# Performance work log

Hardware: AMD Instinct MI355X
Metric: run time of the kernel (lower is better)

Reference implementation:

```python
import jax, jax.numpy as jnp
import numpy as np

B, S, D, H = 1, 2048, 1024, 16
HD = D // H
FF = 4 * D
EPS_LN = 1e-5
EPS_ATTN = 1e-6


def _layernorm(x, g, b):
    mu = jnp.mean(x, axis=-1, keepdims=True)
    var = jnp.mean(jnp.square(x - mu), axis=-1, keepdims=True)
    return (x - mu) * jax.lax.rsqrt(var + EPS_LN) * g + b


def setup_inputs() -> dict:
    key = jax.random.key(0)
    ks = jax.random.split(key, 12)
    w = lambda k, shape: (jax.random.normal(k, shape, jnp.float32) * 0.02)
    return {
        "x": jax.random.normal(ks[0], (B, S, D), jnp.float32),
        "Wq": w(ks[1], (D, D)), "bq": jnp.zeros((D,), jnp.float32),
        "Wk": w(ks[2], (D, D)), "bk": jnp.zeros((D,), jnp.float32),
        "Wv": w(ks[3], (D, D)), "bv": jnp.zeros((D,), jnp.float32),
        "Wo": w(ks[4], (D, D)), "bo": jnp.zeros((D,), jnp.float32),
        "W1": w(ks[5], (FF, D)), "bb1": jnp.zeros((FF,), jnp.float32),
        "W2": w(ks[6], (D, FF)), "bb2": jnp.zeros((D,), jnp.float32),
        "g1": jnp.ones((D,), jnp.float32), "be1": jnp.zeros((D,), jnp.float32),
        "g2": jnp.ones((D,), jnp.float32), "be2": jnp.zeros((D,), jnp.float32),
    }


def reference(x, Wq, bq, Wk, bk, Wv, bv, Wo, bo, W1, bb1, W2, bb2, g1, be1, g2, be2):
    # --- pre-norm causal linear attention ---
    h = _layernorm(x, g1, be1)                     # (B,S,D)
    def heads(t):
        return t.reshape(B, S, H, HD).transpose(0, 2, 1, 3)  # (B,H,S,hd)
    q = heads(h @ Wq.T + bq)
    k = heads(h @ Wk.T + bk)
    v = heads(h @ Wv.T + bv)
    # feature map phi(x) = elu(x) + 1 (strictly positive)
    q = jax.nn.elu(q) + 1.0
    k = jax.nn.elu(k) + 1.0
    # causal cumulative state: S_t = sum_{i<=t} k_i v_i^T ; z_t = sum_{i<=t} k_i
    kv = jnp.cumsum(jnp.einsum("bhsd,bhse->bhsde", k, v), axis=2)  # (B,H,S,hd,hd)
    z = jnp.cumsum(k, axis=2)                                       # (B,H,S,hd)
    num = jnp.einsum("bhsd,bhsde->bhse", q, kv)                    # (B,H,S,hd)
    den = jnp.einsum("bhsd,bhsd->bhs", q, z) + EPS_ATTN
    attn = (num / den[..., None]).transpose(0, 2, 1, 3).reshape(B, S, D)
    attn = attn @ Wo.T + bo
    x = x + attn
    # --- FFN (GELU exact, matching torch nn.GELU default) ---
    h2 = _layernorm(x, g2, be2)
    ff = jax.nn.gelu(h2 @ W1.T + bb1, approximate=False) @ W2.T + bb2
    return x + ff
```

## Files before the change

kernel.cpp:

```cpp
#include <hip/hip_runtime.h>
#include <hip/hip_bf16.h>
#include <math.h>

constexpr int S  = 2048;
constexpr int D  = 1024;
constexpr int H  = 16;
constexpr int HD = 64;
constexpr int FF = 4096;
constexpr int NC  = 32;
constexpr int CHK = 64;
constexpr int QS  = 3 * D;

typedef __attribute__((ext_vector_type(8))) short bf16x8;
typedef __attribute__((ext_vector_type(4))) float f32x4;

__device__ inline unsigned short f2bf(float f) {
    unsigned int u = __float_as_uint(f);
    u = (u + 0x7FFFu + ((u >> 16) & 1u)) >> 16;
    return (unsigned short)u;
}

__global__ __launch_bounds__(256) void cvt_bf16(const float* __restrict__ src,
                                                unsigned short* __restrict__ dst,
                                                int n4) {
    int i = blockIdx.x * 256 + threadIdx.x;
    if (i >= n4) return;
    float4 v = ((const float4*)src)[i];
    ushort4 o = { f2bf(v.x), f2bf(v.y), f2bf(v.z), f2bf(v.w) };
    ((ushort4*)dst)[i] = o;
}

__global__ __launch_bounds__(256) void concat3(const float* __restrict__ a,
                                               const float* __restrict__ b,
                                               const float* __restrict__ c,
                                               float* __restrict__ o) {
    int i = blockIdx.x * 256 + threadIdx.x;
    if (i >= 3 * D) return;
    const float* s = (i < D) ? a : ((i < 2 * D) ? b : c);
    o[i] = s[i & (D - 1)];
}

__global__ __launch_bounds__(256) void layernorm_bf16(const float* __restrict__ x,
                                                      const float* __restrict__ g,
                                                      const float* __restrict__ b,
                                                      unsigned short* __restrict__ out) {
    const int row = blockIdx.x, tid = threadIdx.x;
    float4 v = ((const float4*)(x + (size_t)row * D))[tid];
    float s  = v.x + v.y + v.z + v.w;
    float ss = v.x*v.x + v.y*v.y + v.z*v.z + v.w*v.w;
    #pragma unroll
    for (int off = 32; off > 0; off >>= 1) {
        s  += __shfl_down(s, off);
        ss += __shfl_down(ss, off);
    }
    __shared__ float sw[4], ssw[4];
    if ((tid & 63) == 0) { sw[tid >> 6] = s; ssw[tid >> 6] = ss; }
    __syncthreads();
    s  = sw[0] + sw[1] + sw[2] + sw[3];
    ss = ssw[0] + ssw[1] + ssw[2] + ssw[3];
    const float mu = s * (1.0f / D);
    const float rs = rsqrtf(ss * (1.0f / D) - mu * mu + 1e-5f);
    float4 gv = ((const float4*)g)[tid];
    float4 bv = ((const float4*)b)[tid];
    ushort4 o = { f2bf((v.x - mu) * rs * gv.x + bv.x),
                  f2bf((v.y - mu) * rs * gv.y + bv.y),
                  f2bf((v.z - mu) * rs * gv.z + bv.z),
                  f2bf((v.w - mu) * rs * gv.w + bv.w) };
    ((ushort4*)(out + (size_t)row * D))[tid] = o;
}

enum { EPI_F32 = 0, EPI_QKV = 1, EPI_GELU_BF16 = 2, EPI_PART = 3 };

template <int EPI>
__global__ __launch_bounds__(256) void gemm_bt(const unsigned short* __restrict__ A,
                                               const unsigned short* __restrict__ W,
                                               const float* __restrict__ bias,
                                               void* __restrict__ outp,
                                               int M, int N, int K, int kSplit) {
    __shared__ unsigned short As[128 * 32];
    __shared__ unsigned short Bs[128 * 32];
    const int tid  = threadIdx.x;
    const int tileM = blockIdx.x * 128;
    const int tileN = blockIdx.y * 128;
    const int w    = tid >> 6, lane = tid & 63;
    const int wm   = (w >> 1) * 64, wn = (w & 1) * 64;
    const int lr   = lane & 15, lk = lane >> 4;
    const int kLen   = K / kSplit;
    const int kStart = blockIdx.z * kLen;
    const int kEnd   = kStart + kLen;

    f32x4 acc[4][4];
    #pragma unroll
    for (int i = 0; i < 4; ++i)
        #pragma unroll
        for (int j = 0; j < 4; ++j) acc[i][j] = (f32x4)(0.0f);

    for (int k0 = kStart; k0 < kEnd; k0 += 32) {
        #pragma unroll
        for (int p = 0; p < 2; ++p) {
            const int c   = p * 256 + tid;
            const int row = c >> 2, kc = (c & 3) * 8;
            __builtin_amdgcn_global_load_lds(
                (const __attribute__((address_space(1))) unsigned int*)
                    (A + (size_t)(tileM + row) * K + k0 + kc),
                (__attribute__((address_space(3))) unsigned int*)&As[c * 8],
                16, 0, 0);
            __builtin_amdgcn_global_load_lds(
                (const __attribute__((address_space(1))) unsigned int*)
                    (W + (size_t)(tileN + row) * K + k0 + kc),
                (__attribute__((address_space(3))) unsigned int*)&Bs[c * 8],
                16, 0, 0);
        }
        __syncthreads();
        bf16x8 af[4], bfv[4];
        #pragma unroll
        for (int i = 0; i < 4; ++i) {
            af[i]  = *(const bf16x8*)&As[(wm + i * 16 + lr) * 32 + lk * 8];
            bfv[i] = *(const bf16x8*)&Bs[(wn + i * 16 + lr) * 32 + lk * 8];
        }
        #pragma unroll
        for (int i = 0; i < 4; ++i)
            #pragma unroll
            for (int j = 0; j < 4; ++j)
                acc[i][j] = __builtin_amdgcn_mfma_f32_16x16x32_bf16(af[i], bfv[j], acc[i][j], 0, 0, 0);
        __syncthreads();
    }

    #pragma unroll
    for (int i = 0; i < 4; ++i) {
        const int rbase = tileM + wm + i * 16 + lk * 4;
        #pragma unroll
        for (int j = 0; j < 4; ++j) {
            const int col = tileN + wn + j * 16 + lr;
            #pragma unroll
            for (int r = 0; r < 4; ++r) {
                const int row = rbase + r;
                const size_t off = (size_t)row * N + col;
                float v = acc[i][j][r];
                if constexpr (EPI == EPI_PART) {
                    ((float*)outp)[(size_t)blockIdx.z * (size_t)M * (size_t)N + off] = v;
                } else if constexpr (EPI == EPI_QKV) {
                    v += bias[col];
                    if (col < 2 * D) v = v > 0.0f ? v + 1.0f : __expf(v);
                    ((float*)outp)[off] = v;
                } else if constexpr (EPI == EPI_GELU_BF16) {
                    v += bias[col];
                    float gl = 0.5f * v * (1.0f + erff(v * 0.70710678118654752f));
                    ((unsigned short*)outp)[off] = f2bf(gl);
                } else {
                    v += bias[col];
                    ((float*)outp)[off] = v;
                }
            }
        }
    }
}

__global__ __launch_bounds__(256) void reduce_bias_res(const float* __restrict__ part,
                                                       const float* __restrict__ bias,
                                                       const float* __restrict__ res,
                                                       float* __restrict__ out,
                                                       int N4, int total4, int KS) {
    int i = blockIdx.x * 256 + threadIdx.x;
    if (i >= total4) return;
    float4 a = ((const float4*)part)[i];
    for (int z = 1; z < KS; ++z) {
        float4 p = ((const float4*)part)[(size_t)z * total4 + i];
        a.x += p.x; a.y += p.y; a.z += p.z; a.w += p.w;
    }
    float4 b = ((const float4*)bias)[i % N4];
    float4 r = ((const float4*)res)[i];
    a.x += b.x + r.x; a.y += b.y + r.y; a.z += b.z + r.z; a.w += b.w + r.w;
    ((float4*)out)[i] = a;
}

__global__ __launch_bounds__(256) void attn_chunk_sums(const float* __restrict__ qkv,
                                                       float* __restrict__ KVc,
                                                       float* __restrict__ Zc) {
    const int c = blockIdx.x, h = blockIdx.y, tid = threadIdx.x;
    __shared__ float Kc[CHK * HD], Vc[CHK * HD];
    const int s0 = c * CHK;
    #pragma unroll
    for (int p = 0; p < 4; ++p) {
        int cc = p * 256 + tid;
        int t = cc >> 4, dp = (cc & 15) * 4;
        *(float4*)&Kc[t * HD + dp] = *(const float4*)(qkv + (size_t)(s0 + t) * QS + D     + h * HD + dp);
        *(float4*)&Vc[t * HD + dp] = *(const float4*)(qkv + (size_t)(s0 + t) * QS + 2 * D + h * HD + dp);
    }
    __syncthreads();
    const int d = tid >> 2, e0 = (tid & 3) * 16;
    float acc[16];
    #pragma unroll
    for (int j = 0; j < 16; ++j) acc[j] = 0.0f;
    float zacc = 0.0f;
    for (int t = 0; t < CHK; ++t) {
        float kv = Kc[t * HD + d];
        zacc += kv;
        #pragma unroll
        for (int j = 0; j < 16; ++j) acc[j] += kv * Vc[t * HD + e0 + j];
    }
    float* op = KVc + ((size_t)(h * NC + c) * HD + d) * HD + e0;
    #pragma unroll
    for (int j = 0; j < 16; ++j) op[j] = acc[j];
    if ((tid & 3) == 0) Zc[(size_t)(h * NC + c) * HD + d] = zacc;
}

__global__ __launch_bounds__(256) void attn_prefix(float* __restrict__ KVc,
                                                   float* __restrict__ Zc) {
    const int h = blockIdx.y;
    const int elem = blockIdx.x * 256 + threadIdx.x;
    size_t base = (size_t)h * NC * (HD * HD) + elem;
    float run = 0.0f;
    for (int c = 0; c < NC; ++c) {
        float t = KVc[base + (size_t)c * (HD * HD)];
        KVc[base + (size_t)c * (HD * HD)] = run;
        run += t;
    }
    if (blockIdx.x == 0 && threadIdx.x < HD) {
        size_t zb = (size_t)h * NC * HD + threadIdx.x;
        float zr = 0.0f;
        for (int c = 0; c < NC; ++c) {
            float t = Zc[zb + (size_t)c * HD];
            Zc[zb + (size_t)c * HD] = zr;
            zr += t;
        }
    }
}

__global__ __launch_bounds__(256) void attn_out(const float* __restrict__ qkv,
                                                const float* __restrict__ KVpre,
                                                const float* __restrict__ Zpre,
                                                unsigned short* __restrict__ attn) {
    const int c = blockIdx.x, h = blockIdx.y, tid = threadIdx.x;
    __shared__ float Qc[CHK * HD], KVs[CHK * HD], Pre[HD * HD], Sc[CHK * CHK];
    __shared__ float zp[HD], den[CHK];
    const int s0 = c * CHK;
    #pragma unroll
    for (int p = 0; p < 4; ++p) {
        int cc = p * 256 + tid;
        int t = cc >> 4, dp = (cc & 15) * 4;
        *(float4*)&Qc[t * HD + dp]  = *(const float4*)(qkv + (size_t)(s0 + t) * QS +     h * HD + dp);
        *(float4*)&KVs[t * HD + dp] = *(const float4*)(qkv + (size_t)(s0 + t) * QS + D + h * HD + dp);
        ((float4*)Pre)[cc] = *(const float4*)(KVpre + (size_t)(h * NC + c) * (HD * HD) + cc * 4);
    }
    if (tid < HD) zp[tid] = Zpre[(size_t)(h * NC + c) * HD + tid];
    __syncthreads();

    const int tt = tid >> 2, i0 = (tid & 3) * 16;
    for (int i = i0; i < i0 + 16; ++i) {
        float sv = 0.0f;
        for (int d2 = 0; d2 < HD; ++d2) sv += Qc[tt * HD + d2] * KVs[i * HD + d2];
        Sc[tt * CHK + i] = (i <= tt) ? sv : 0.0f;
    }
    __syncthreads();

    if (tid < CHK) {
        float dv = 1e-6f;
        for (int d2 = 0; d2 < HD; ++d2) dv += Qc[tid * HD + d2] * zp[d2];
        for (int i = 0; i < CHK; ++i) dv += Sc[tid * CHK + i];
        den[tid] = dv;
    }
    #pragma unroll
    for (int p = 0; p < 4; ++p) {
        int cc = p * 256 + tid;
        int t = cc >> 4, dp = (cc & 15) * 4;
        *(float4*)&KVs[t * HD + dp] = *(const float4*)(qkv + (size_t)(s0 + t) * QS + 2 * D + h * HD + dp);
    }
    __syncthreads();

    float o[16];
    #pragma unroll
    for (int j = 0; j < 16; ++j) o[j] = 0.0f;
    for (int d2 = 0; d2 < HD; ++d2) {
        float qv = Qc[tt * HD + d2];
        float sv = Sc[tt * CHK + d2];
        #pragma unroll
        for (int j = 0; j < 16; ++j)
            o[j] += qv * Pre[d2 * HD + i0 + j] + sv * KVs[d2 * HD + i0 + j];
    }
    const float inv = 1.0f / den[tt];
    unsigned short* op = attn + (size_t)(s0 + tt) * D + h * HD + i0;
    #pragma unroll
    for (int j0 = 0; j0 < 16; j0 += 4) {
        ushort4 ov = { f2bf(o[j0] * inv), f2bf(o[j0 + 1] * inv),
                       f2bf(o[j0 + 2] * inv), f2bf(o[j0 + 3] * inv) };
        *(ushort4*)(op + j0) = ov;
    }
}

extern "C" void kernel_launch(void* const* d_in, const int* in_sizes, int n_in,
                              void* d_out, int out_size, void* d_ws, size_t ws_size,
                              hipStream_t stream) {
    const float* x   = (const float*)d_in[0];
    const float* Wq  = (const float*)d_in[1];
    const float* bq  = (const float*)d_in[2];
    const float* Wk  = (const float*)d_in[3];
    const float* bk  = (const float*)d_in[4];
    const float* Wv  = (const float*)d_in[5];
    const float* bv  = (const float*)d_in[6];
    const float* Wo  = (const float*)d_in[7];
    const float* bo  = (const float*)d_in[8];
    const float* W1  = (const float*)d_in[9];
    const float* b1  = (const float*)d_in[10];
    const float* W2  = (const float*)d_in[11];
    const float* b2  = (const float*)d_in[12];
    const float* g1  = (const float*)d_in[13];
    const float* be1 = (const float*)d_in[14];
    const float* g2  = (const float*)d_in[15];
    const float* be2 = (const float*)d_in[16];
    float* out = (float*)d_out;

    char* wsp = (char*)d_ws;
    auto alloc = [&](size_t bytes) {
        char* p = wsp;
        wsp += (bytes + 255) & ~(size_t)255;
        return p;
    };
    unsigned short* h1   = (unsigned short*)alloc((size_t)S * D * 2);
    unsigned short* attn = (unsigned short*)alloc((size_t)S * D * 2);
    unsigned short* gbuf = (unsigned short*)alloc((size_t)S * FF * 2);
    float* x2   = (float*)alloc((size_t)S * D * 4);
    unsigned short* Wqkvb = (unsigned short*)alloc((size_t)3 * D * D * 2);
    unsigned short* Wob   = (unsigned short*)alloc((size_t)D * D * 2);
    unsigned short* W1b   = (unsigned short*)alloc((size_t)FF * D * 2);
    unsigned short* W2b   = (unsigned short*)alloc((size_t)D * FF * 2);
    float* bqkv = (float*)alloc((size_t)3 * D * 4);
    float* KVc  = (float*)alloc((size_t)H * NC * HD * HD * 4);
    float* Zc   = (float*)alloc((size_t)H * NC * HD * 4);
    char* uni = (char*)alloc((size_t)32 * 1024 * 1024);
    float* qkv   = (float*)uni;
    float* parts = (float*)uni;

    const int DD4 = D * D / 4, FD4 = FF * D / 4;
    cvt_bf16<<<DD4 / 256, 256, 0, stream>>>(Wq, Wqkvb,             DD4);
    cvt_bf16<<<DD4 / 256, 256, 0, stream>>>(Wk, Wqkvb + D * D,     DD4);
    cvt_bf16<<<DD4 / 256, 256, 0, stream>>>(Wv, Wqkvb + 2 * D * D, DD4);
    cvt_bf16<<<DD4 / 256, 256, 0, stream>>>(Wo, Wob, DD4);
    cvt_bf16<<<FD4 / 256, 256, 0, stream>>>(W1, W1b, FD4);
    cvt_bf16<<<FD4 / 256, 256, 0, stream>>>(W2, W2b, FD4);
    concat3<<<(3 * D + 255) / 256, 256, 0, stream>>>(bq, bk, bv, bqkv);

    layernorm_bf16<<<S, 256, 0, stream>>>(x, g1, be1, h1);

    gemm_bt<EPI_QKV><<<dim3(S / 128, 3 * D / 128, 1), 256, 0, stream>>>(
        h1, Wqkvb, bqkv, qkv, S, 3 * D, D, 1);

    attn_chunk_sums<<<dim3(NC, H), 256, 0, stream>>>(qkv, KVc, Zc);
    attn_prefix<<<dim3(16, H), 256, 0, stream>>>(KVc, Zc);
    attn_out<<<dim3(NC, H), 256, 0, stream>>>(qkv, KVc, Zc, attn);

    gemm_bt<EPI_PART><<<dim3(S / 128, D / 128, 2), 256, 0, stream>>>(
        attn, Wob, nullptr, parts, S, D, D, 2);
    reduce_bias_res<<<(S * D / 4 + 255) / 256, 256, 0, stream>>>(
        parts, bo, x, x2, D / 4, S * D / 4, 2);

    layernorm_bf16<<<S, 256, 0, stream>>>(x2, g2, be2, h1);

    gemm_bt<EPI_GELU_BF16><<<dim3(S / 128, FF / 128, 1), 256, 0, stream>>>(
        h1, W1b, b1, gbuf, S, FF, D, 1);

    gemm_bt<EPI_PART><<<dim3(S / 128, D / 128, 4), 256, 0, stream>>>(
        gbuf, W2b, nullptr, parts, S, D, FF, 4);
    reduce_bias_res<<<(S * D / 4 + 255) / 256, 256, 0, stream>>>(
        parts, b2, x2, out, D / 4, S * D / 4, 4);
}
```

Measured before the change: 319.5 us.

## Merge weight conversions, fuse residual reduce with layernorm, use 512-thread GEMM blocks

Six weight-conversion launches and the bias concat are replaced by one kernel, and the QKV bias is now chosen per column in the epilogue. The split-K reduce after the output projection is fused with the second layernorm, which removes one kernel and one pass over x2. The GEMM moves to 512 threads in 8 waves, each wave owning a 64x32 sub-tile, which halves accumulator registers and lets each thread issue one LDS load per operand. Launch overhead and memory traffic drop, but per-wave MFMA work is smaller, so A-fragment reuse per wave is lower.

```diff
diff --git a/kernel.cpp b/kernel.cpp
--- a/kernel.cpp
+++ b/kernel.cpp
@@ -20,24 +20,33 @@
     return (unsigned short)u;
 }
 
-__global__ __launch_bounds__(256) void cvt_bf16(const float* __restrict__ src,
-                                                unsigned short* __restrict__ dst,
-                                                int n4) {
+constexpr int DD4 = D * D / 4;
+constexpr int FD4 = FF * D / 4;
+constexpr int CVT_TOTAL4 = 4 * DD4 + 2 * FD4;
+
+__global__ __launch_bounds__(256) void cvt6(const float* __restrict__ Wq,
+                                            const float* __restrict__ Wk,
+                                            const float* __restrict__ Wv,
+                                            const float* __restrict__ Wo,
+                                            const float* __restrict__ W1,
+                                            const float* __restrict__ W2,
+                                            unsigned short* __restrict__ Wqkvb,
+                                            unsigned short* __restrict__ Wob,
+                                            unsigned short* __restrict__ W1b,
+                                            unsigned short* __restrict__ W2b) {
     int i = blockIdx.x * 256 + threadIdx.x;
-    if (i >= n4) return;
-    float4 v = ((const float4*)src)[i];
+    if (i >= CVT_TOTAL4) return;
+    const float* s;
+    unsigned short* dp;
+    if (i < DD4)                 { s = Wq + (size_t)i * 4;               dp = Wqkvb + (size_t)i * 4; }
+    else if (i < 2 * DD4)        { s = Wk + (size_t)(i - DD4) * 4;       dp = Wqkvb + (size_t)i * 4; }
+    else if (i < 3 * DD4)        { s = Wv + (size_t)(i - 2 * DD4) * 4;   dp = Wqkvb + (size_t)i * 4; }
+    else if (i < 4 * DD4)        { s = Wo + (size_t)(i - 3 * DD4) * 4;   dp = Wob + (size_t)(i - 3 * DD4) * 4; }
+    else if (i < 4 * DD4 + FD4)  { s = W1 + (size_t)(i - 4 * DD4) * 4;   dp = W1b + (size_t)(i - 4 * DD4) * 4; }
+    else                         { s = W2 + (size_t)(i - 4 * DD4 - FD4) * 4; dp = W2b + (size_t)(i - 4 * DD4 - FD4) * 4; }
+    float4 v = *(const float4*)s;
     ushort4 o = { f2bf(v.x), f2bf(v.y), f2bf(v.z), f2bf(v.w) };
-    ((ushort4*)dst)[i] = o;
-}
-
-__global__ __launch_bounds__(256) void concat3(const float* __restrict__ a,
-                                               const float* __restrict__ b,
-                                               const float* __restrict__ c,
-                                               float* __restrict__ o) {
-    int i = blockIdx.x * 256 + threadIdx.x;
-    if (i >= 3 * D) return;
-    const float* s = (i < D) ? a : ((i < 2 * D) ? b : c);
-    o[i] = s[i & (D - 1)];
+    *(ushort4*)dp = o;
 }
 
 __global__ __launch_bounds__(256) void layernorm_bf16(const float* __restrict__ x,
@@ -69,59 +78,121 @@
     ((ushort4*)(out + (size_t)row * D))[tid] = o;
 }
 
+template <int KS>
+__global__ __launch_bounds__(256) void reduce_ln(const float* __restrict__ part,
+                                                 const float* __restrict__ bias,
+                                                 const float* __restrict__ res,
+                                                 float* __restrict__ x2,
+                                                 const float* __restrict__ g,
+                                                 const float* __restrict__ b,
+                                                 unsigned short* __restrict__ out) {
+    const int row = blockIdx.x, tid = threadIdx.x;
+    const size_t i4 = (size_t)row * 256 + tid;
+    float4 a = ((const float4*)part)[i4];
+    #pragma unroll
+    for (int z = 1; z < KS; ++z) {
+        float4 p = ((const float4*)part)[(size_t)z * S * 256 + i4];
+        a.x += p.x; a.y += p.y; a.z += p.z; a.w += p.w;
+    }
+    float4 bi = ((const float4*)bias)[tid];
+    float4 r  = ((const float4*)res)[i4];
+    a.x += bi.x + r.x; a.y += bi.y + r.y; a.z += bi.z + r.z; a.w += bi.w + r.w;
+    ((float4*)x2)[i4] = a;
+    float s  = a.x + a.y + a.z + a.w;
+    float ss = a.x*a.x + a.y*a.y + a.z*a.z + a.w*a.w;
+    #pragma unroll
+    for (int off = 32; off > 0; off >>= 1) {
+        s  += __shfl_down(s, off);
+        ss += __shfl_down(ss, off);
+    }
+    __shared__ float sw[4], ssw[4];
+    if ((tid & 63) == 0) { sw[tid >> 6] = s; ssw[tid >> 6] = ss; }
+    __syncthreads();
+    s  = sw[0] + sw[1] + sw[2] + sw[3];
+    ss = ssw[0] + ssw[1] + ssw[2] + ssw[3];
+    const float mu = s * (1.0f / D);
+    const float rs = rsqrtf(ss * (1.0f / D) - mu * mu + 1e-5f);
+    float4 gv = ((const float4*)g)[tid];
+    float4 bv = ((const float4*)b)[tid];
+    ushort4 o = { f2bf((a.x - mu) * rs * gv.x + bv.x),
+                  f2bf((a.y - mu) * rs * gv.y + bv.y),
+                  f2bf((a.z - mu) * rs * gv.z + bv.z),
+                  f2bf((a.w - mu) * rs * gv.w + bv.w) };
+    ((ushort4*)(out + (size_t)row * D))[tid] = o;
+}
+
+template <int KS>
+__global__ __launch_bounds__(256) void reduce_bias_res(const float* __restrict__ part,
+                                                       const float* __restrict__ bias,
+                                                       const float* __restrict__ res,
+                                                       float* __restrict__ out,
+                                                       int N4, int total4) {
+    int i = blockIdx.x * 256 + threadIdx.x;
+    if (i >= total4) return;
+    float4 a = ((const float4*)part)[i];
+    #pragma unroll
+    for (int z = 1; z < KS; ++z) {
+        float4 p = ((const float4*)part)[(size_t)z * total4 + i];
+        a.x += p.x; a.y += p.y; a.z += p.z; a.w += p.w;
+    }
+    float4 b = ((const float4*)bias)[i % N4];
+    float4 r = ((const float4*)res)[i];
+    a.x += b.x + r.x; a.y += b.y + r.y; a.z += b.z + r.z; a.w += b.w + r.w;
+    ((float4*)out)[i] = a;
+}
+
 enum { EPI_F32 = 0, EPI_QKV = 1, EPI_GELU_BF16 = 2, EPI_PART = 3 };
 
 template <int EPI>
-__global__ __launch_bounds__(256) void gemm_bt(const unsigned short* __restrict__ A,
-                                               const unsigned short* __restrict__ W,
-                                               const float* __restrict__ bias,
-                                               void* __restrict__ outp,
-                                               int M, int N, int K, int kSplit) {
+__global__ __launch_bounds__(512, 4) void gemm_bt(const unsigned short* __restrict__ A,
+                                                  const unsigned short* __restrict__ W,
+                                                  const float* __restrict__ bias,
+                                                  const float* __restrict__ bias2,
+                                                  const float* __restrict__ bias3,
+                                                  void* __restrict__ outp,
+                                                  int M, int N, int K, int kSplit) {
     __shared__ unsigned short As[128 * 32];
     __shared__ unsigned short Bs[128 * 32];
     const int tid  = threadIdx.x;
     const int tileM = blockIdx.x * 128;
     const int tileN = blockIdx.y * 128;
     const int w    = tid >> 6, lane = tid & 63;
-    const int wm   = (w >> 1) * 64, wn = (w & 1) * 64;
+    const int wm   = (w >> 2) * 64, wn = (w & 3) * 32;
     const int lr   = lane & 15, lk = lane >> 4;
     const int kLen   = K / kSplit;
     const int kStart = blockIdx.z * kLen;
     const int kEnd   = kStart + kLen;
-
-    f32x4 acc[4][4];
+    const int srow = tid >> 2, skc = (tid & 3) * 8;
+
+    f32x4 acc[4][2];
     #pragma unroll
     for (int i = 0; i < 4; ++i)
         #pragma unroll
-        for (int j = 0; j < 4; ++j) acc[i][j] = (f32x4)(0.0f);
+        for (int j = 0; j < 2; ++j) acc[i][j] = (f32x4)(0.0f);
 
     for (int k0 = kStart; k0 < kEnd; k0 += 32) {
-        #pragma unroll
-        for (int p = 0; p < 2; ++p) {
-            const int c   = p * 256 + tid;
-            const int row = c >> 2, kc = (c & 3) * 8;
-            __builtin_amdgcn_global_load_lds(
-                (const __attribute__((address_space(1))) unsigned int*)
-                    (A + (size_t)(tileM + row) * K + k0 + kc),
-                (__attribute__((address_space(3))) unsigned int*)&As[c * 8],
-                16, 0, 0);
-            __builtin_amdgcn_global_load_lds(
-                (const __attribute__((address_space(1))) unsigned int*)
-                    (W + (size_t)(tileN + row) * K + k0 + kc),
-                (__attribute__((address_space(3))) unsigned int*)&Bs[c * 8],
-                16, 0, 0);
-        }
+        __builtin_amdgcn_global_load_lds(
+            (const __attribute__((address_space(1))) unsigned int*)
+                (A + (size_t)(tileM + srow) * K + k0 + skc),
+            (__attribute__((address_space(3))) unsigned int*)&As[tid * 8],
+            16, 0, 0);
+        __builtin_amdgcn_global_load_lds(
+            (const __attribute__((address_space(1))) unsigned int*)
+                (W + (size_t)(tileN + srow) * K + k0 + skc),
+            (__attribute__((address_space(3))) unsigned int*)&Bs[tid * 8],
+            16, 0, 0);
         __syncthreads();
-        bf16x8 af[4], bfv[4];
-        #pragma unroll
-        for (int i = 0; i < 4; ++i) {
+        bf16x8 af[4], bfv[2];
+        #pragma unroll
+        for (int i = 0; i < 4; ++i)
             af[i]  = *(const bf16x8*)&As[(wm + i * 16 + lr) * 32 + lk * 8];
-            bfv[i] = *(const bf16x8*)&Bs[(wn + i * 16 + lr) * 32 + lk * 8];
-        }
+        #pragma unroll
+        for (int j = 0; j < 2; ++j)
+            bfv[j] = *(const bf16x8*)&Bs[(wn + j * 16 + lr) * 32 + lk * 8];
         #pragma unroll
         for (int i = 0; i < 4; ++i)
             #pragma unroll
-            for (int j = 0; j < 4; ++j)
+            for (int j = 0; j < 2; ++j)
                 acc[i][j] = __builtin_amdgcn_mfma_f32_16x16x32_bf16(af[i], bfv[j], acc[i][j], 0, 0, 0);
         __syncthreads();
     }
@@ -130,7 +201,7 @@
     for (int i = 0; i < 4; ++i) {
         const int rbase = tileM + wm + i * 16 + lk * 4;
         #pragma unroll
-        for (int j = 0; j < 4; ++j) {
+        for (int j = 0; j < 2; ++j) {
             const int col = tileN + wn + j * 16 + lr;
             #pragma unroll
             for (int r = 0; r < 4; ++r) {
@@ -140,7 +211,8 @@
                 if constexpr (EPI == EPI_PART) {
                     ((float*)outp)[(size_t)blockIdx.z * (size_t)M * (size_t)N + off] = v;
                 } else if constexpr (EPI == EPI_QKV) {
-                    v += bias[col];
+                    float bc = (col < D) ? bias[col] : ((col < 2 * D) ? bias2[col - D] : bias3[col - 2 * D]);
+                    v += bc;
                     if (col < 2 * D) v = v > 0.0f ? v + 1.0f : __expf(v);
                     ((float*)outp)[off] = v;
                 } else if constexpr (EPI == EPI_GELU_BF16) {
@@ -154,24 +226,6 @@
             }
         }
     }
-}
-
-__global__ __launch_bounds__(256) void reduce_bias_res(const float* __restrict__ part,
-                                                       const float* __restrict__ bias,
-                                                       const float* __restrict__ res,
-                                                       float* __restrict__ out,
-                                                       int N4, int total4, int KS) {
-    int i = blockIdx.x * 256 + threadIdx.x;
-    if (i >= total4) return;
-    float4 a = ((const float4*)part)[i];
-    for (int z = 1; z < KS; ++z) {
-        float4 p = ((const float4*)part)[(size_t)z * total4 + i];
-        a.x += p.x; a.y += p.y; a.z += p.z; a.w += p.w;
-    }
-    float4 b = ((const float4*)bias)[i % N4];
-    float4 r = ((const float4*)res)[i];
-    a.x += b.x + r.x; a.y += b.y + r.y; a.z += b.z + r.z; a.w += b.w + r.w;
-    ((float4*)out)[i] = a;
 }
 
 __global__ __launch_bounds__(256) void attn_chunk_sums(const float* __restrict__ qkv,
@@ -324,43 +378,33 @@
     unsigned short* Wob   = (unsigned short*)alloc((size_t)D * D * 2);
     unsigned short* W1b   = (unsigned short*)alloc((size_t)FF * D * 2);
     unsigned short* W2b   = (unsigned short*)alloc((size_t)D * FF * 2);
-    float* bqkv = (float*)alloc((size_t)3 * D * 4);
     float* KVc  = (float*)alloc((size_t)H * NC * HD * HD * 4);
     float* Zc   = (float*)alloc((size_t)H * NC * HD * 4);
     char* uni = (char*)alloc((size_t)32 * 1024 * 1024);
     float* qkv   = (float*)uni;
     float* parts = (float*)uni;
 
-    const int DD4 = D * D / 4, FD4 = FF * D / 4;
-    cvt_bf16<<<DD4 / 256, 256, 0, stream>>>(Wq, Wqkvb,             DD4);
-    cvt_bf16<<<DD4 / 256, 256, 0, stream>>>(Wk, Wqkvb + D * D,     DD4);
-    cvt_bf16<<<DD4 / 256, 256, 0, stream>>>(Wv, Wqkvb + 2 * D * D, DD4);
-    cvt_bf16<<<DD4 / 256, 256, 0, stream>>>(Wo, Wob, DD4);
-    cvt_bf16<<<FD4 / 256, 256, 0, stream>>>(W1, W1b, FD4);
-    cvt_bf16<<<FD4 / 256, 256, 0, stream>>>(W2, W2b, FD4);
-    concat3<<<(3 * D + 255) / 256, 256, 0, stream>>>(bq, bk, bv, bqkv);
+    cvt6<<<(CVT_TOTAL4 + 255) / 256, 256, 0, stream>>>(Wq, Wk, Wv, Wo, W1, W2,
+                                                       Wqkvb, Wob, W1b, W2b);
 
     layernorm_bf16<<<S, 256, 0, stream>>>(x, g1, be1, h1);
 
-    gemm_bt<EPI_QKV><<<dim3(S / 128, 3 * D / 128, 1), 256, 0, stream>>>(
-        h1, Wqkvb, bqkv, qkv, S, 3 * D, D, 1);
+    gemm_bt<EPI_QKV><<<dim3(S / 128, 3 * D / 128, 1), 512, 0, stream>>>(
+        h1, Wqkvb, bq, bk, bv, qkv, S, 3 * D, D, 1);
 
     attn_chunk_sums<<<dim3(NC, H), 256, 0, stream>>>(qkv, KVc, Zc);
     attn_prefix<<<dim3(16, H), 256, 0, stream>>>(KVc, Zc);
     attn_out<<<dim3(NC, H), 256, 0, stream>>>(qkv, KVc, Zc, attn);
 
-    gemm_bt<EPI_PART><<<dim3(S / 128, D / 128, 2), 256, 0, stream>>>(
-        attn, Wob, nullptr, parts, S, D, D, 2);
-    reduce_bias_res<<<(S * D / 4 + 255) / 256, 256, 0, stream>>>(
-        parts, bo, x, x2, D / 4, S * D / 4, 2);
-
-    layernorm_bf16<<<S, 256, 0, stream>>>(x2, g2, be2, h1);
-
-    gemm_bt<EPI_GELU_BF16><<<dim3(S / 128, FF / 128, 1), 256, 0, stream>>>(
-        h1, W1b, b1, gbuf, S, FF, D, 1);
-
-    gemm_bt<EPI_PART><<<dim3(S / 128, D / 128, 4), 256, 0, stream>>>(
-        gbuf, W2b, nullptr, parts, S, D, FF, 4);
-    reduce_bias_res<<<(S * D / 4 + 255) / 256, 256, 0, stream>>>(
-        parts, b2, x2, out, D / 4, S * D / 4, 4);
-}
+    gemm_bt<EPI_PART><<<dim3(S / 128, D / 128, 2), 512, 0, stream>>>(
+        attn, Wob, nullptr, nullptr, nullptr, parts, S, D, D, 2);
+    reduce_ln<2><<<S, 256, 0, stream>>>(parts, bo, x, x2, g2, be2, h1);
+
+    gemm_bt<EPI_GELU_BF16><<<dim3(S / 128, FF / 128, 1), 512, 0, stream>>>(
+        h1, W1b, b1, nullptr, nullptr, gbuf, S, FF, D, 1);
+
+    gemm_bt<EPI_PART><<<dim3(S / 128, D / 128, 4), 512, 0, stream>>>(
+        gbuf, W2b, nullptr, nullptr, nullptr, parts, S, D, FF, 4);
+    reduce_bias_res<4><<<(S * D / 4 + 255) / 256, 256, 0, stream>>>(
+        parts, b2, x2, out, D / 4, S * D / 4);
+}
```

Result: faster. 291.6 us (-8.7%).
